# Kernel tuning notes

Measured on AMD Instinct MI355X. Metric: run time of the kernel, lower is better.

## Reference

```python
import jax, jax.numpy as jnp
import numpy as np


def _igd(x, pf):
    # pf: [M, d] reference front, x: [N, d] candidate set
    # squared Euclidean distances via ||a||^2 + ||b||^2 - 2 a.b (cdist expansion)
    pf_sq = jnp.sum(pf * pf, axis=1, keepdims=True)          # [M, 1]
    x_sq = jnp.sum(x * x, axis=1, keepdims=True).T            # [1, N]
    cross = pf @ x.T                                          # [M, N]
    d2 = jnp.maximum(pf_sq + x_sq - 2.0 * cross, 0.0)
    dist = jnp.sqrt(d2)                                       # [M, N]
    # IGD: mean over reference points of min distance to candidate set
    return jnp.mean(jnp.min(dist, axis=1))


def setup_inputs() -> dict:
    key = jax.random.key(0)
    k1, k2 = jax.random.split(key)
    N, M, D = 16384, 16384, 64
    x = jax.random.normal(k1, (N, D), dtype=jnp.float32)
    pf = jax.random.normal(k2, (M, D), dtype=jnp.float32)
    return {"x": x, "pf": pf}


def reference(x, pf):
    return _igd(x, pf)
```

## Files before the change

kernel.cpp:

```cpp
#include <hip/hip_runtime.h>


typedef float f32x16 __attribute__((ext_vector_type(16)));
typedef float f32x2 __attribute__((ext_vector_type(2)));
typedef int i32x8 __attribute__((ext_vector_type(8)));
typedef unsigned long long u64;

#define DIM 64
#define NSPLIT 16
#define UNITB 2048
#define MTILE 256

union BFrag { u64 q[4]; i32x8 v; };

__device__ __forceinline__ void encode16(const float* f, u64 w[2], float& sumsq) {
    unsigned int w32[4];
#pragma unroll
    for (int k = 0; k < 4; ++k) {
        int lo = __builtin_amdgcn_cvt_pk_fp8_f32(f[4 * k],     f[4 * k + 1], 0,  false);
        w32[k] = __builtin_amdgcn_cvt_pk_fp8_f32(f[4 * k + 2], f[4 * k + 3], lo, true);
    }
#pragma unroll
    for (int k = 0; k < 4; ++k) {
        f32x2 d0 = __builtin_amdgcn_cvt_pk_f32_fp8(w32[k], false);
        f32x2 d1 = __builtin_amdgcn_cvt_pk_f32_fp8(w32[k], true);
        sumsq += d0.x * d0.x + d0.y * d0.y + d1.x * d1.x + d1.y * d1.y;
    }
    w[0] = (u64)w32[0] | ((u64)w32[1] << 32);
    w[1] = (u64)w32[2] | ((u64)w32[3] << 32);
}

__global__ void pack_kernel(const float* __restrict__ x, const float* __restrict__ pf,
                            unsigned char* __restrict__ Bp, unsigned char* __restrict__ Ab,
                            float* __restrict__ xsq, float* __restrict__ pfsq,
                            float* __restrict__ out, int N, int M) {
    int gid = blockIdx.x * blockDim.x + threadIdx.x;
    if (gid == 0) out[0] = 0.f;
    if (gid < N * 4) {
        int col = gid >> 2, t = gid & 3;
        const float* s = x + (size_t)col * DIM + t * 16;
        float4 v0 = *(const float4*)(s);
        float4 v1 = *(const float4*)(s + 4);
        float4 v2 = *(const float4*)(s + 8);
        float4 v3 = *(const float4*)(s + 12);
        float f[16] = {v0.x, v0.y, v0.z, v0.w, v1.x, v1.y, v1.z, v1.w,
                       v2.x, v2.y, v2.z, v2.w, v3.x, v3.y, v3.z, v3.w};
        float partial = 0.f;
        u64 w[2];
        encode16(f, w, partial);
        int u = col >> 5, c31 = col & 31;
        unsigned char* ub = Bp + (size_t)u * UNITB;
        int h = t >> 1;
#pragma unroll
        for (int ss = 0; ss < 2; ++ss) {
            int q = (t & 1) * 2 + ss;
            *(u64*)(ub + (size_t)q * 512 + (size_t)(h * 32 + c31) * 8) = w[ss];
        }
        partial += __shfl_xor(partial, 1);
        partial += __shfl_xor(partial, 2);
        if (t == 0) xsq[col] = partial;
    } else {
        int g = gid - N * 4;
        int row = g >> 2, q = g & 3;
        if (row >= M) return;
        const float* s = pf + (size_t)row * DIM + q * 16;
        float4 v0 = *(const float4*)(s);
        float4 v1 = *(const float4*)(s + 4);
        float4 v2 = *(const float4*)(s + 8);
        float4 v3 = *(const float4*)(s + 12);
        float f[16] = {v0.x, v0.y, v0.z, v0.w, v1.x, v1.y, v1.z, v1.w,
                       v2.x, v2.y, v2.z, v2.w, v3.x, v3.y, v3.z, v3.w};
#pragma unroll
        for (int j = 0; j < 16; ++j) f[j] *= -2.f;
        float partial = 0.f;
        u64 w[2];
        encode16(f, w, partial);
        *(u64*)(Ab + (size_t)row * DIM + q * 16)     = w[0];
        *(u64*)(Ab + (size_t)row * DIM + q * 16 + 8) = w[1];
        partial += __shfl_xor(partial, 1);
        partial += __shfl_xor(partial, 2);
        if (q == 0) pfsq[row] = partial * 0.25f;
    }
}

__global__ __launch_bounds__(256, 4)
void igd_main(const unsigned char* __restrict__ A, const unsigned char* __restrict__ Bp,
              const float* __restrict__ xsq, float* __restrict__ partial, int N) {
    const int tid = threadIdx.x;
    const int mTile  = blockIdx.x;
    const int nsplit = blockIdx.y;
    const int lane = tid & 63;
    const int wave = tid >> 6;
    const int half = lane >> 5;
    const int l31  = lane & 31;
    const int rowBase = mTile * MTILE + wave * 64;

    const int utotal = N / 32;
    const int ubase  = utotal / NSPLIT;
    const int urem   = utotal % NSPLIT;
    const int ustart = nsplit * ubase + (nsplit < urem ? nsplit : urem);
    const int ucount = ubase + (nsplit < urem ? 1 : 0);

    BFrag a[2];
#pragma unroll
    for (int g = 0; g < 2; ++g) {
        const unsigned char* ap = A + (size_t)(rowBase + 32 * g + l31) * DIM + half * 32;
#pragma unroll
        for (int qq = 0; qq < 4; ++qq)
            a[g].q[qq] = *(const u64*)(ap + qq * 8);
    }

    const unsigned char* bG = Bp + (size_t)ustart * UNITB + lane * 8;
    const float* xG = xsq + ustart * 32 + l31;

#define LOADG(rr, u)                                                           \
    {                                                                          \
        const unsigned char* p = bG + (size_t)(u) * UNITB;                     \
        rr.q[0] = *(const u64*)(p);                                            \
        rr.q[1] = *(const u64*)(p + 512);                                      \
        rr.q[2] = *(const u64*)(p + 1024);                                     \
        rr.q[3] = *(const u64*)(p + 1536);                                     \
    }

    f32x16 zero, m0, m1;
#pragma unroll
    for (int r = 0; r < 16; ++r) { zero[r] = 0.f; m0[r] = 1e30f; m1[r] = 1e30f; }

#define MFMA2(accA, accB, bfrag)                                               \
    {                                                                          \
        accA = __builtin_amdgcn_mfma_scale_f32_32x32x64_f8f6f4(                \
            a[0].v, bfrag.v, zero, 0, 0, 0, 0x7F7F7F7F, 0, 0x7F7F7F7F);        \
        accB = __builtin_amdgcn_mfma_scale_f32_32x32x64_f8f6f4(                \
            a[1].v, bfrag.v, zero, 0, 0, 0, 0x7F7F7F7F, 0, 0x7F7F7F7F);        \
    }

#define MINS(accA, accB, xq0)                                                  \
    {                                                                          \
        _Pragma("unroll")                                                      \
        for (int r = 0; r < 16; ++r) {                                         \
            m0[r] = fminf(m0[r], accA[r] + (xq0));                             \
            m1[r] = fminf(m1[r], accB[r] + (xq0));                             \
        }                                                                      \
    }

    BFrag b[2];
    float xq[2];
#pragma unroll
    for (int i = 0; i < 2; ++i) {
        LOADG(b[i], i);
        xq[i] = xG[(size_t)i * 32];
    }

    const int umain = ucount & ~1;
    for (int u = 0; u < umain; u += 2) {
#pragma unroll
        for (int s = 0; s < 2; ++s) {
            f32x16 acA, acB;
            MFMA2(acA, acB, b[s]);
            const float x0 = xq[s];
            LOADG(b[s], u + 2 + s);
            xq[s] = xG[(size_t)(u + 2 + s) * 32];
            MINS(acA, acB, x0);
        }
    }
    if (umain < ucount) {
        f32x16 acA, acB;
        MFMA2(acA, acB, b[0]);
        MINS(acA, acB, xq[0]);
    }
#undef LOADG
#undef MFMA2
#undef MINS

#pragma unroll
    for (int mask = 1; mask <= 16; mask <<= 1) {
#pragma unroll
        for (int r = 0; r < 16; ++r) {
            m0[r] = fminf(m0[r], __shfl_xor(m0[r], mask));
            m1[r] = fminf(m1[r], __shfl_xor(m1[r], mask));
        }
    }
    if (l31 == 0) {
#pragma unroll
        for (int r = 0; r < 16; ++r) {
            int row0 = rowBase + (r & 3) + 8 * (r >> 2) + 4 * half;
            partial[(size_t)row0 * NSPLIT + nsplit] = m0[r];
            partial[(size_t)(row0 + 32) * NSPLIT + nsplit] = m1[r];
        }
    }
}

__global__ void reduce_kernel(const float* __restrict__ partial, const float* __restrict__ pfsq,
                              float* __restrict__ out, int M, float invM) {
    int row = blockIdx.x * blockDim.x + threadIdx.x;
    float v = 0.f;
    if (row < M) {
        const float* p = partial + (size_t)row * NSPLIT;
        float mn = 3.4e38f;
#pragma unroll
        for (int s = 0; s < NSPLIT; ++s) mn = fminf(mn, p[s]);
        float d2 = mn + pfsq[row];
        v = sqrtf(fmaxf(d2, 0.f)) * invM;
    }
#pragma unroll
    for (int m = 1; m < 64; m <<= 1) v += __shfl_xor(v, m);
    __shared__ float wsum[4];
    int lane = threadIdx.x & 63, w = threadIdx.x >> 6;
    if (lane == 0) wsum[w] = v;
    __syncthreads();
    if (threadIdx.x == 0) atomicAdd(out, wsum[0] + wsum[1] + wsum[2] + wsum[3]);
}

extern "C" void kernel_launch(void* const* d_in, const int* in_sizes, int n_in,
                              void* d_out, int out_size, void* d_ws, size_t ws_size,
                              hipStream_t stream) {
    const float* x  = (const float*)d_in[0];
    const float* pf = (const float*)d_in[1];
    const int N = in_sizes[0] / DIM;
    const int M = in_sizes[1] / DIM;

    char* ws = (char*)d_ws;
    unsigned char* Bp = (unsigned char*)ws;
    unsigned char* Ab = (unsigned char*)(ws + (size_t)N * DIM);
    float* xsq  = (float*)(ws + (size_t)(N + M) * DIM);
    float* pfsq = xsq + N;
    float* part = pfsq + M;

    int packThreads = (N + M) * 4;
    pack_kernel<<<dim3((packThreads + 255) / 256), 256, 0, stream>>>(
        x, pf, Bp, Ab, xsq, pfsq, (float*)d_out, N, M);
    igd_main<<<dim3(M / MTILE, NSPLIT), 256, 0, stream>>>(Ab, Bp, xsq, part, N);
    reduce_kernel<<<dim3((M + 255) / 256), 256, 0, stream>>>(part, pfsq, (float*)d_out, M, 1.f / (float)M);
}
```

Before: 90.73 us.

## Software-pipeline MFMA with min-reduction and retune split count and occupancy

Restructures the main loop so the MFMA for the next unit is issued before the min-reduction of the previous unit's accumulators, using double-buffered accumulator registers. This lets the matrix-core work overlap with the VALU fminf work. The extra accumulators raise register pressure, so launch bounds drop from 4 to 3 blocks per SM, and NSPLIT goes from 16 to 12 so the grid fits the new occupancy. The risk is lower occupancy hiding less memory latency.

Result: faster. 88.73 us (-2.2%).

```diff
diff --git a/kernel.cpp b/kernel.cpp
--- a/kernel.cpp
+++ b/kernel.cpp
@@ -7,7 +7,7 @@
 typedef unsigned long long u64;
 
 #define DIM 64
-#define NSPLIT 16
+#define NSPLIT 12
 #define UNITB 2048
 #define MTILE 256
 
@@ -83,7 +83,7 @@
     }
 }
 
-__global__ __launch_bounds__(256, 4)
+__global__ __launch_bounds__(256, 3)
 void igd_main(const unsigned char* __restrict__ A, const unsigned char* __restrict__ Bp,
               const float* __restrict__ xsq, float* __restrict__ partial, int N) {
     const int tid = threadIdx.x;
@@ -134,39 +134,44 @@
             a[1].v, bfrag.v, zero, 0, 0, 0, 0x7F7F7F7F, 0, 0x7F7F7F7F);        \
     }
 
-#define MINS(accA, accB, xq0)                                                  \
+#define MINS(p0, p1, xx)                                                       \
     {                                                                          \
         _Pragma("unroll")                                                      \
         for (int r = 0; r < 16; ++r) {                                         \
-            m0[r] = fminf(m0[r], accA[r] + (xq0));                             \
-            m1[r] = fminf(m1[r], accB[r] + (xq0));                             \
+            m0[r] = fminf(m0[r], p0[r] + (xx));                                \
+            m1[r] = fminf(m1[r], p1[r] + (xx));                                \
         }                                                                      \
     }
 
     BFrag b[2];
     float xq[2];
-#pragma unroll
-    for (int i = 0; i < 2; ++i) {
-        LOADG(b[i], i);
-        xq[i] = xG[(size_t)i * 32];
-    }
-
-    const int umain = ucount & ~1;
-    for (int u = 0; u < umain; u += 2) {
-#pragma unroll
-        for (int s = 0; s < 2; ++s) {
-            f32x16 acA, acB;
-            MFMA2(acA, acB, b[s]);
-            const float x0 = xq[s];
-            LOADG(b[s], u + 2 + s);
-            xq[s] = xG[(size_t)(u + 2 + s) * 32];
-            MINS(acA, acB, x0);
-        }
-    }
-    if (umain < ucount) {
-        f32x16 acA, acB;
-        MFMA2(acA, acB, b[0]);
-        MINS(acA, acB, xq[0]);
+    LOADG(b[0], 0); xq[0] = xG[0];
+    LOADG(b[1], 1); xq[1] = xG[32];
+
+    f32x16 pX0, pX1, pY0, pY1;
+    float xX, xY;
+
+    MFMA2(pY0, pY1, b[0]);
+    xY = xq[0];
+    LOADG(b[0], 2); xq[0] = xG[(size_t)2 * 32];
+
+    const int pairs = (ucount - 1) / 2;
+    for (int g = 0; g < pairs; ++g) {
+        const int u = 1 + 2 * g;
+        MFMA2(pX0, pX1, b[1]);
+        xX = xq[1];
+        LOADG(b[1], u + 2); xq[1] = xG[(size_t)(u + 2) * 32];
+        MINS(pY0, pY1, xY);
+        MFMA2(pY0, pY1, b[0]);
+        xY = xq[0];
+        LOADG(b[0], u + 3); xq[0] = xG[(size_t)(u + 3) * 32];
+        MINS(pX0, pX1, xX);
+    }
+    MINS(pY0, pY1, xY);
+    if (2 * pairs + 1 < ucount) {
+        f32x16 tA, tB;
+        MFMA2(tA, tB, b[1]);
+        MINS(tA, tB, xq[1]);
     }
 #undef LOADG
 #undef MFMA2
```
